# Kernel tuning notes

Hardware: AMD Instinct MI355X
Metric: run time of the kernel (lower is better)

Reference implementation:

```python
import jax, jax.numpy as jnp
import numpy as np

B, S, T, L, D, H = 32, 64, 256, 8, 128, 128
SIGNAL_SD = 1.0 - 0.001   # default signal_sds init
NOISE_SD = 0.01           # GP diagonal jitter (noise_sds) for Cholesky stability


def setup_inputs() -> dict:
    key = jax.random.key(0)
    ks = jax.random.split(key, 8)
    X = jax.random.normal(ks[0], (B, T, D), dtype=jnp.float32)
    times = (jnp.arange(T, dtype=jnp.float32) / T) * 10.0  # span [0, 10)
    log_taus = jax.random.normal(ks[1], (L,), dtype=jnp.float32) * 0.1 + jnp.log(0.5)
    log_R_diag = jax.random.normal(ks[2], (D,), dtype=jnp.float32) * 0.1
    W1 = jax.random.normal(ks[3], (L, H), dtype=jnp.float32) / np.sqrt(L)
    b1 = jnp.zeros((H,), dtype=jnp.float32)
    W2 = jax.random.normal(ks[4], (H, D), dtype=jnp.float32) / np.sqrt(H)
    b2 = jnp.zeros((D,), dtype=jnp.float32)
    eps = jax.random.normal(ks[5], (B, S, L, T), dtype=jnp.float32)
    return {"X": X, "times": times, "log_taus": log_taus, "log_R_diag": log_R_diag,
            "W1": W1, "b1": b1, "W2": W2, "b2": b2, "eps": eps}


def reference(X, times, log_taus, log_R_diag, W1, b1, W2, b2, eps):
    taus = jnp.exp(log_taus)            # [L]
    r = jnp.exp(log_R_diag)             # [D] diagonal of R

    # --- GP prior kernel matrices (squared-exponential SDE kernel), one per latent dim ---
    dt = times[:, None] - times[None, :]                       # [T,T]
    K = (SIGNAL_SD ** 2) * jnp.exp(-(dt ** 2)[None] / (2.0 * (taus ** 2)[:, None, None]))
    K = K + (NOISE_SD ** 2) * jnp.eye(T, dtype=K.dtype)        # [L,T,T]
    Lc = jnp.linalg.cholesky(K)                                # [L,T,T]

    # --- reparameterized prior samples: z = Lc @ eps ---
    z = jnp.einsum('lut,bslt->bslu', Lc, eps)                  # [B,S,L,T]
    Z = jnp.transpose(z, (0, 1, 3, 2))                         # [B,S,T,L]

    # --- decoder MLP: latent -> manifold mean in observation space ---
    h = jnp.tanh(jnp.einsum('bstl,lh->bsth', Z, W1) + b1)      # [B,S,T,H]
    mu = jnp.einsum('bsth,hd->bstd', h, W2) + b2               # [B,S,T,D]

    # --- diagonal-R Gaussian log_prob per timestep, closed form ---
    diff = X[:, None, :, :] - mu                               # [B,S,T,D]
    quad = jnp.sum(diff * diff / r, axis=-1)                   # [B,S,T]
    log_norm = 0.5 * (jnp.sum(log_R_diag) + D * jnp.log(2.0 * jnp.pi))
    logp = -0.5 * quad - log_norm                              # [B,S,T]

    # --- sum over time, logsumexp over MC samples ---
    ll = jnp.sum(logp, axis=2)                                 # [B,S]
    nll = -(jax.scipy.special.logsumexp(ll, axis=1) - jnp.log(jnp.float32(S)))
    return nll                                                 # [B]
```

## Files before the change

kernel.cpp:

```cpp
#include <hip/hip_runtime.h>
#include <hip/hip_bf16.h>
#include <math.h>

#define B_ 32
#define S_ 64
#define T_ 256
#define L_ 8
#define D_ 128
#define H_ 128

typedef __attribute__((ext_vector_type(8))) short short8;
typedef __attribute__((ext_vector_type(4))) short short4v;
typedef __attribute__((ext_vector_type(4))) float float4v;

__device__ __forceinline__ short f2bf(float x) {
  __hip_bfloat16 h = __float2bfloat16(x);
  return *reinterpret_cast<short*>(&h);
}

__device__ __forceinline__ float rdlane(float x, int sl) {
  return __int_as_float(__builtin_amdgcn_readlane(__float_as_int(x), sl));
}
__device__ __forceinline__ float dpp_shr1(float x, float tailv) {
  int r = __builtin_amdgcn_update_dpp(__float_as_int(tailv), __float_as_int(x),
                                      0x138, 0xF, 0xF, false);
  return __int_as_float(r);
}

__global__ __launch_bounds__(64) void k_chol_prep(
    const float* __restrict__ times, const float* __restrict__ log_taus,
    __hip_bfloat16* __restrict__ Lcbf_,
    const float* __restrict__ W1, const float* __restrict__ W2,
    __hip_bfloat16* __restrict__ W1T, __hip_bfloat16* __restrict__ W2T)
{
  __shared__ short panel[256][68];
  const int bi = blockIdx.x;
  const int j = threadIdx.x;

  if (bi >= 8) {
    const int base = (bi - 8) * 64 + j;
    for (int idx = base; idx < H_ * D_; idx += 4096) {
      const int cc = idx >> 7, h = idx & 127;
      const int n = cc & 15, nt = cc >> 4;
      const int d = n * 8 + nt;
      W2T[(size_t)cc * H_ + h] = __float2bfloat16(W2[(size_t)h * D_ + d]);
    }
    for (int idx = base; idx < L_ * H_; idx += 4096) {
      const int li = idx >> 7, h = idx & 127;
      W1T[(size_t)h * L_ + li] = __float2bfloat16(W1[idx]);
    }
    return;
  }

  const int l = bi;
  short* Lbf = (short*)Lcbf_ + (size_t)l * T_ * T_;

  const float tau = expf(log_taus[l]);
  const float inv2tau2 = 0.5f / (tau * tau);
  const float sig2 = 0.999f * 0.999f;
  const float t0 = times[0];

  const float c0 = sig2 + 1e-4f;
  const float isc0 = 1.0f / sqrtf(c0);

  float u[4], v[4];
#pragma unroll
  for (int c = 0; c < 4; ++c) {
    const int d = c * 64 + j;
    const float dt = times[d] - t0;
    float cv = sig2 * __expf(-dt * dt * inv2tau2);
    if (d == 0) cv = c0;
    u[c] = cv * isc0;
    v[c] = (d == 0) ? 0.0f : u[c];
  }

#pragma unroll
  for (int p = 0; p < 4; ++p) {
    for (int kk = 0; kk < 64; ++kk) {
      const float uk = rdlane(u[p], kk);
      const float vk = rdlane(v[p], kk);
      const float rho = vk * __builtin_amdgcn_rcpf(uk);
      const float om = fmaxf(1.0f - rho * rho, 1e-12f);
      const float s = __builtin_amdgcn_rsqf(om);
      const float sr = s * rho;

      float up[4];
#pragma unroll
      for (int c = 0; c < 4; ++c) {
        if (c >= p) {
          const float uc = u[c], vc = v[c];
          up[c] = s * uc - sr * vc;
          v[c]  = s * vc - sr * uc;
          const float val = (c > p || j >= kk) ? up[c] : 0.0f;
          panel[(c - p) * 64 + j][kk] = f2bf(val);
        }
      }
#pragma unroll
      for (int c = 3; c >= 0; --c) {
        if (c >= p) {
          const float tail = (c > p) ? rdlane(up[c - 1], 63) : 0.0f;
          u[c] = dpp_shr1(up[c], tail);
        }
      }
    }
    __syncthreads();
    const int rpt = 256 - 64 * p;
    const int rsub = j >> 4, cp = (j & 15) * 4;
    for (int i0 = 0; i0 < rpt; i0 += 4) {
      const int pr = i0 + rsub;
      short4v vv = *(const short4v*)&panel[pr][cp];
      *(short4v*)&Lbf[((size_t)(p * 64 + pr) << 8) + p * 64 + cp] = vv;
    }
    __syncthreads();
  }
}

__global__ __launch_bounds__(256) void k_zgemm(
    const float* __restrict__ eps, const __hip_bfloat16* __restrict__ Lcbf_,
    __hip_bfloat16* __restrict__ Zg)
{
  __shared__ __align__(16) short E[64][264];
  const int bi = blockIdx.x;
  const int l = bi & 7, bs0 = (bi >> 3) * 64;
  const int tid = threadIdx.x, w = tid >> 6, lane = tid & 63;
  const int n = lane & 15, q = lane >> 4;
  const short* Lb = (const short*)Lcbf_ + (size_t)l * T_ * T_;

  {
    const int row = tid >> 2, seg = (tid & 3) * 64;
    const float* src = eps + ((size_t)(bs0 + row) * L_ + l) * T_ + seg;
#pragma unroll
    for (int g = 0; g < 16; ++g) {
      float4v f = *(const float4v*)(src + g * 4);
      short4v o;
#pragma unroll
      for (int jj = 0; jj < 4; ++jj) o[jj] = f2bf(f[jj]);
      *(short4v*)&E[row][seg + g * 4] = o;
    }
  }
  __syncthreads();

  float4v acc[4][4];
#pragma unroll
  for (int mt = 0; mt < 4; ++mt)
#pragma unroll
    for (int nt = 0; nt < 4; ++nt) acc[mt][nt] = (float4v){0.f, 0.f, 0.f, 0.f};

  const int kend = (w + 1) * 64;
  for (int k0 = 0; k0 < kend; k0 += 32) {
    short8 bfrg[4], afr[4];
#pragma unroll
    for (int nt = 0; nt < 4; ++nt)
      bfrg[nt] = *(const short8*)&E[nt * 16 + n][k0 + q * 8];
#pragma unroll
    for (int mt = 0; mt < 4; ++mt) {
      const int u = w * 64 + mt * 16 + n;
      afr[mt] = *(const short8*)&Lb[((size_t)u << 8) + k0 + q * 8];
    }
#pragma unroll
    for (int mt = 0; mt < 4; ++mt)
#pragma unroll
      for (int nt = 0; nt < 4; ++nt)
        acc[mt][nt] = __builtin_amdgcn_mfma_f32_16x16x32_bf16(afr[mt], bfrg[nt], acc[mt][nt], 0, 0, 0);
  }
#pragma unroll
  for (int mt = 0; mt < 4; ++mt)
#pragma unroll
    for (int nt = 0; nt < 4; ++nt) {
      const int bs = bs0 + nt * 16 + n;
#pragma unroll
      for (int r = 0; r < 4; ++r) {
        const int u = w * 64 + mt * 16 + q * 4 + r;
        Zg[((size_t)bs << 11) + (u << 3) + l] = __float2bfloat16(acc[mt][nt][r]);
      }
    }
}

__global__ __launch_bounds__(256, 4) void k_decode(
    const float* __restrict__ X, const __hip_bfloat16* __restrict__ Zg,
    const __hip_bfloat16* __restrict__ W1T, const float* __restrict__ b1,
    const __hip_bfloat16* __restrict__ W2T, const float* __restrict__ b2,
    const float* __restrict__ log_R, float* __restrict__ ll)
{
  __shared__ __align__(16) short Zt[256][8];
  __shared__ __align__(16) __hip_bfloat16 hS[128][136];
  __shared__ float redbuf[4];

  const int bs = blockIdx.x;
  const int b = bs >> 6;
  const int tid = threadIdx.x;
  const int w = tid >> 6, lane = tid & 63;
  const int n = lane & 15, q = lane >> 4;
  const short* Zs = (const short*)Zg;
  const short* W1s = (const short*)W1T;
  const short* W2s = (const short*)W2T;

  *(short8*)&Zt[tid][0] = *(const short8*)&Zs[((size_t)bs << 11) + tid * 8];

  float sLR = log_R[lane] + log_R[lane + 64];
#pragma unroll
  for (int off = 32; off >= 1; off >>= 1) sLR += __shfl_xor(sLR, off);

  const int d0 = n * 8 + 2 * w;
  float invr2[2], b22[2], b12[2];
#pragma unroll
  for (int jj = 0; jj < 2; ++jj) {
    invr2[jj] = expf(-log_R[d0 + jj]);
    b22[jj] = b2[d0 + jj];
    b12[jj] = b1[(2 * w + jj) * 16 + n];
  }

  const short8 zero8 = {0, 0, 0, 0, 0, 0, 0, 0};
  short8 w1f[2];
  short8 bfr[2][4];
#pragma unroll
  for (int jj = 0; jj < 2; ++jj) {
    const int c = (2 * w + jj) * 16 + n;
    short8 v = zero8;
    if (q == 0) v = *(const short8*)&W1s[(size_t)c * L_];
    w1f[jj] = v;
#pragma unroll
    for (int ks = 0; ks < 4; ++ks)
      bfr[jj][ks] = *(const short8*)&W2s[(size_t)c * H_ + ks * 32 + q * 8];
  }

  float qsum = 0.0f;
  __syncthreads();

#pragma unroll 1
  for (int half = 0; half < 2; ++half) {
#pragma unroll 1
    for (int mi = 0; mi < 8; ++mi) {
      short8 zf = zero8;
      if (q == 0) zf = *(const short8*)&Zt[half * 128 + mi * 16 + n][0];
      float4v c0 = __builtin_amdgcn_mfma_f32_16x16x32_bf16(zf, w1f[0], (float4v){0.f,0.f,0.f,0.f}, 0, 0, 0);
      float4v c1 = __builtin_amdgcn_mfma_f32_16x16x32_bf16(zf, w1f[1], (float4v){0.f,0.f,0.f,0.f}, 0, 0, 0);
#pragma unroll
      for (int r = 0; r < 4; ++r) {
        float a0 = c0[r] + b12[0];
        float a1 = c1[r] + b12[1];
        float p0 = __expf(2.f * a0) + 1.f;
        float p1 = __expf(2.f * a1) + 1.f;
        float rj = __builtin_amdgcn_rcpf(p0 * p1);
        float h0 = 1.f - 2.f * p1 * rj;
        float h1 = 1.f - 2.f * p0 * rj;
        hS[mi * 16 + q * 4 + r][(2 * w) * 16 + n] = __float2bfloat16(h0);
        hS[mi * 16 + q * 4 + r][(2 * w + 1) * 16 + n] = __float2bfloat16(h1);
      }
    }
    __syncthreads();
#pragma unroll 1
    for (int mi = 0; mi < 8; ++mi) {
      short8 af[4];
#pragma unroll
      for (int ks = 0; ks < 4; ++ks)
        af[ks] = *(const short8*)&hS[mi * 16 + n][ks * 32 + q * 8];
      float4v acc0 = (float4v){0.f, 0.f, 0.f, 0.f};
      float4v acc1 = (float4v){0.f, 0.f, 0.f, 0.f};
#pragma unroll
      for (int ks = 0; ks < 4; ++ks) {
        acc0 = __builtin_amdgcn_mfma_f32_16x16x32_bf16(af[ks], bfr[0][ks], acc0, 0, 0, 0);
        acc1 = __builtin_amdgcn_mfma_f32_16x16x32_bf16(af[ks], bfr[1][ks], acc1, 0, 0, 0);
      }
#pragma unroll
      for (int r = 0; r < 4; ++r) {
        const int t = half * 128 + mi * 16 + q * 4 + r;
        const float2 xv = *(const float2*)(X + (((size_t)b << 8) + t) * D_ + d0);
        float diff0 = xv.x - (acc0[r] + b22[0]);
        float diff1 = xv.y - (acc1[r] + b22[1]);
        qsum += diff0 * diff0 * invr2[0] + diff1 * diff1 * invr2[1];
      }
    }
    __syncthreads();
  }

#pragma unroll
  for (int off = 32; off >= 1; off >>= 1) qsum += __shfl_xor(qsum, off);
  if (lane == 0) redbuf[w] = qsum;
  __syncthreads();
  if (tid == 0) {
    float Q = redbuf[0] + redbuf[1] + redbuf[2] + redbuf[3];
    float log_norm = 0.5f * (sLR + (float)D_ * 1.8378770664093453f);
    ll[bs] = -0.5f * Q - (float)T_ * log_norm;
  }
}

__global__ __launch_bounds__(64) void k_lse(
    const float* __restrict__ ll, float* __restrict__ out)
{
  const int b = blockIdx.x;
  const int s = threadIdx.x;
  float v = ll[b * 64 + s];
  float m = v;
#pragma unroll
  for (int off = 32; off >= 1; off >>= 1) m = fmaxf(m, __shfl_xor(m, off));
  float e = __expf(v - m);
#pragma unroll
  for (int off = 32; off >= 1; off >>= 1) e += __shfl_xor(e, off);
  if (s == 0) out[b] = -(m + __logf(e) - 4.1588830833596715f);
}

extern "C" void kernel_launch(void* const* d_in, const int* in_sizes, int n_in,
                              void* d_out, int out_size, void* d_ws, size_t ws_size,
                              hipStream_t stream) {
  const float* X        = (const float*)d_in[0];
  const float* times    = (const float*)d_in[1];
  const float* log_taus = (const float*)d_in[2];
  const float* log_R    = (const float*)d_in[3];
  const float* W1       = (const float*)d_in[4];
  const float* b1       = (const float*)d_in[5];
  const float* W2       = (const float*)d_in[6];
  const float* b2       = (const float*)d_in[7];
  const float* eps      = (const float*)d_in[8];
  float* out = (float*)d_out;

  char* ws = (char*)d_ws;
  __hip_bfloat16* Lcbf = (__hip_bfloat16*)(ws);
  __hip_bfloat16* Zg   = (__hip_bfloat16*)(ws + 1048576);
  float* ll            = (float*)(ws + 9437184);
  __hip_bfloat16* W2T  = (__hip_bfloat16*)(ws + 9445376);
  __hip_bfloat16* W1T  = (__hip_bfloat16*)(ws + 9478144);

  hipLaunchKernelGGL(k_chol_prep, dim3(72),   dim3(64),  0, stream,
                     times, log_taus, Lcbf, W1, W2, W1T, W2T);
  hipLaunchKernelGGL(k_zgemm,     dim3(256),  dim3(256), 0, stream, eps, Lcbf, Zg);
  hipLaunchKernelGGL(k_decode,    dim3(2048), dim3(256), 0, stream, X, Zg, W1T, b1, W2T, b2, log_R, ll);
  hipLaunchKernelGGL(k_lse,       dim3(32),   dim3(64),  0, stream, ll, out);
}
```

Measured before the change: 173.5 us.

## Fuse logsumexp into decode via last-block atomic counter; halve zgemm tile

After: 231.4 us. +33.4%, slower.

```diff
diff --git a/kernel.cpp b/kernel.cpp
--- a/kernel.cpp
+++ b/kernel.cpp
@@ -31,13 +31,15 @@
     const float* __restrict__ times, const float* __restrict__ log_taus,
     __hip_bfloat16* __restrict__ Lcbf_,
     const float* __restrict__ W1, const float* __restrict__ W2,
-    __hip_bfloat16* __restrict__ W1T, __hip_bfloat16* __restrict__ W2T)
+    __hip_bfloat16* __restrict__ W1T, __hip_bfloat16* __restrict__ W2T,
+    unsigned* __restrict__ cnt)
 {
   __shared__ short panel[256][68];
   const int bi = blockIdx.x;
   const int j = threadIdx.x;
 
   if (bi >= 8) {
+    if (bi == 8 && j < B_) cnt[j] = 0;
     const int base = (bi - 8) * 64 + j;
     for (int idx = base; idx < H_ * D_; idx += 4096) {
       const int cc = idx >> 7, h = idx & 127;
@@ -119,18 +121,18 @@
     const float* __restrict__ eps, const __hip_bfloat16* __restrict__ Lcbf_,
     __hip_bfloat16* __restrict__ Zg)
 {
-  __shared__ __align__(16) short E[64][264];
+  __shared__ __align__(16) short E[32][264];
   const int bi = blockIdx.x;
-  const int l = bi & 7, bs0 = (bi >> 3) * 64;
+  const int l = bi & 7, bs0 = (bi >> 3) * 32;
   const int tid = threadIdx.x, w = tid >> 6, lane = tid & 63;
   const int n = lane & 15, q = lane >> 4;
   const short* Lb = (const short*)Lcbf_ + (size_t)l * T_ * T_;
 
   {
-    const int row = tid >> 2, seg = (tid & 3) * 64;
+    const int row = tid >> 3, seg = (tid & 7) * 32;
     const float* src = eps + ((size_t)(bs0 + row) * L_ + l) * T_ + seg;
 #pragma unroll
-    for (int g = 0; g < 16; ++g) {
+    for (int g = 0; g < 8; ++g) {
       float4v f = *(const float4v*)(src + g * 4);
       short4v o;
 #pragma unroll
@@ -140,17 +142,17 @@
   }
   __syncthreads();
 
-  float4v acc[4][4];
+  float4v acc[4][2];
 #pragma unroll
   for (int mt = 0; mt < 4; ++mt)
 #pragma unroll
-    for (int nt = 0; nt < 4; ++nt) acc[mt][nt] = (float4v){0.f, 0.f, 0.f, 0.f};
+    for (int nt = 0; nt < 2; ++nt) acc[mt][nt] = (float4v){0.f, 0.f, 0.f, 0.f};
 
   const int kend = (w + 1) * 64;
   for (int k0 = 0; k0 < kend; k0 += 32) {
-    short8 bfrg[4], afr[4];
-#pragma unroll
-    for (int nt = 0; nt < 4; ++nt)
+    short8 bfrg[2], afr[4];
+#pragma unroll
+    for (int nt = 0; nt < 2; ++nt)
       bfrg[nt] = *(const short8*)&E[nt * 16 + n][k0 + q * 8];
 #pragma unroll
     for (int mt = 0; mt < 4; ++mt) {
@@ -160,13 +162,13 @@
 #pragma unroll
     for (int mt = 0; mt < 4; ++mt)
 #pragma unroll
-      for (int nt = 0; nt < 4; ++nt)
+      for (int nt = 0; nt < 2; ++nt)
         acc[mt][nt] = __builtin_amdgcn_mfma_f32_16x16x32_bf16(afr[mt], bfrg[nt], acc[mt][nt], 0, 0, 0);
   }
 #pragma unroll
   for (int mt = 0; mt < 4; ++mt)
 #pragma unroll
-    for (int nt = 0; nt < 4; ++nt) {
+    for (int nt = 0; nt < 2; ++nt) {
       const int bs = bs0 + nt * 16 + n;
 #pragma unroll
       for (int r = 0; r < 4; ++r) {
@@ -180,11 +182,13 @@
     const float* __restrict__ X, const __hip_bfloat16* __restrict__ Zg,
     const __hip_bfloat16* __restrict__ W1T, const float* __restrict__ b1,
     const __hip_bfloat16* __restrict__ W2T, const float* __restrict__ b2,
-    const float* __restrict__ log_R, float* __restrict__ ll)
+    const float* __restrict__ log_R, float* __restrict__ ll,
+    unsigned* __restrict__ cnt, float* __restrict__ out)
 {
   __shared__ __align__(16) short Zt[256][8];
   __shared__ __align__(16) __hip_bfloat16 hS[128][136];
   __shared__ float redbuf[4];
+  __shared__ int lastflag;
 
   const int bs = blockIdx.x;
   const int b = bs >> 6;
@@ -281,23 +285,24 @@
   if (tid == 0) {
     float Q = redbuf[0] + redbuf[1] + redbuf[2] + redbuf[3];
     float log_norm = 0.5f * (sLR + (float)D_ * 1.8378770664093453f);
-    ll[bs] = -0.5f * Q - (float)T_ * log_norm;
-  }
-}
-
-__global__ __launch_bounds__(64) void k_lse(
-    const float* __restrict__ ll, float* __restrict__ out)
-{
-  const int b = blockIdx.x;
-  const int s = threadIdx.x;
-  float v = ll[b * 64 + s];
-  float m = v;
-#pragma unroll
-  for (int off = 32; off >= 1; off >>= 1) m = fmaxf(m, __shfl_xor(m, off));
-  float e = __expf(v - m);
-#pragma unroll
-  for (int off = 32; off >= 1; off >>= 1) e += __shfl_xor(e, off);
-  if (s == 0) out[b] = -(m + __logf(e) - 4.1588830833596715f);
+    float llv = -0.5f * Q - (float)T_ * log_norm;
+    __hip_atomic_store(&ll[bs], llv, __ATOMIC_RELEASE, __HIP_MEMORY_SCOPE_AGENT);
+    unsigned old = __hip_atomic_fetch_add(&cnt[b], 1u, __ATOMIC_ACQ_REL,
+                                          __HIP_MEMORY_SCOPE_AGENT);
+    lastflag = (old == S_ - 1) ? 1 : 0;
+  }
+  __syncthreads();
+  if (lastflag && tid < 64) {
+    float v = __hip_atomic_load(&ll[b * 64 + tid], __ATOMIC_RELAXED,
+                                __HIP_MEMORY_SCOPE_AGENT);
+    float m = v;
+#pragma unroll
+    for (int off = 32; off >= 1; off >>= 1) m = fmaxf(m, __shfl_xor(m, off));
+    float e = __expf(v - m);
+#pragma unroll
+    for (int off = 32; off >= 1; off >>= 1) e += __shfl_xor(e, off);
+    if (tid == 0) out[b] = -(m + __logf(e) - 4.1588830833596715f);
+  }
 }
 
 extern "C" void kernel_launch(void* const* d_in, const int* in_sizes, int n_in,
@@ -320,10 +325,11 @@
   float* ll            = (float*)(ws + 9437184);
   __hip_bfloat16* W2T  = (__hip_bfloat16*)(ws + 9445376);
   __hip_bfloat16* W1T  = (__hip_bfloat16*)(ws + 9478144);
+  unsigned* cnt        = (unsigned*)(ws + 9480192);
 
   hipLaunchKernelGGL(k_chol_prep, dim3(72),   dim3(64),  0, stream,
-                     times, log_taus, Lcbf, W1, W2, W1T, W2T);
-  hipLaunchKernelGGL(k_zgemm,     dim3(256),  dim3(256), 0, stream, eps, Lcbf, Zg);
-  hipLaunchKernelGGL(k_decode,    dim3(2048), dim3(256), 0, stream, X, Zg, W1T, b1, W2T, b2, log_R, ll);
-  hipLaunchKernelGGL(k_lse,       dim3(32),   dim3(64),  0, stream, ll, out);
-}
+                     times, log_taus, Lcbf, W1, W2, W1T, W2T, cnt);
+  hipLaunchKernelGGL(k_zgemm,     dim3(512),  dim3(256), 0, stream, eps, Lcbf, Zg);
+  hipLaunchKernelGGL(k_decode,    dim3(2048), dim3(256), 0, stream,
+                     X, Zg, W1T, b1, W2T, b2, log_R, ll, cnt, out);
+}
```
